# Kernel tuning notes

Measured on AMD Instinct MI355X. Metric: run time of the kernel, lower is better.

Reference implementation:

```python
import jax, jax.numpy as jnp
import numpy as np


def setup_inputs() -> dict:
    key = jax.random.key(0)
    kq, kk, kv = jax.random.split(key, 3)
    B, H, S, D = 2, 8, 2048, 64
    Q = jax.random.normal(kq, (B, H, S, D), dtype=jnp.float32)
    K = jax.random.normal(kk, (B, 1, S, D), dtype=jnp.float32)
    V = jax.random.normal(kv, (B, 1, S, D), dtype=jnp.float32)
    return {"Q": Q, "K": K, "V": V}


def reference(Q, K, V):
    # Multi-query attention: K/V have a single shared head.
    D = Q.shape[-1]
    scale = 1.0 / jnp.sqrt(jnp.asarray(D, dtype=Q.dtype))
    Kh = K[:, 0]  # [B, S, D]
    Vh = V[:, 0]  # [B, S, D]
    # scores: [B, H, Sq, Sk]
    scores = jnp.einsum('bhqd,bkd->bhqk', Q, Kh) * scale
    probs = jax.nn.softmax(scores, axis=-1)
    out = jnp.einsum('bhqk,bkd->bhqd', probs, Vh)  # [B, H, S, D]
    return out
```

## Files before the change

kernel.cpp:

```cpp
#include <hip/hip_runtime.h>
#include <stdint.h>

typedef __attribute__((ext_vector_type(8))) short     bf16x8;
typedef __attribute__((ext_vector_type(4))) float     f32x4;
typedef __attribute__((ext_vector_type(4))) float     float4v;
typedef __attribute__((ext_vector_type(2))) unsigned  uint2v;
typedef __attribute__((ext_vector_type(4))) unsigned  uint4v;

#define DEVINL static __device__ __forceinline__

#define B_  2
#define H_  8
#define S_  2048
#define D_  64
#define KVB 128
#define NKT (S_ / KVB)

DEVINL unsigned short f2bf(float f) {
  union { float f; unsigned u; } v; v.f = f;
  unsigned r = v.u + 0x7FFFu + ((v.u >> 16) & 1u);
  return (unsigned short)(r >> 16);
}

DEVINL void gload_lds16(const void* g, void* l) {
  __builtin_amdgcn_global_load_lds(
      (const __attribute__((address_space(1))) void*)g,
      (__attribute__((address_space(3))) void*)l, 16, 0, 0);
}

__global__ __launch_bounds__(256) void prep_kernel(
    const float* __restrict__ K, const float* __restrict__ V,
    unsigned short* __restrict__ Kb, unsigned short* __restrict__ Vt) {
  const int t = threadIdx.x;
  if (blockIdx.x < 128) {
    const int base = blockIdx.x * 2048 + t * 8;
    const float4v a = *(const float4v*)(K + base);
    const float4v b = *(const float4v*)(K + base + 4);
    uint4v o;
    o.x = (unsigned)f2bf(a.x) | ((unsigned)f2bf(a.y) << 16);
    o.y = (unsigned)f2bf(a.z) | ((unsigned)f2bf(a.w) << 16);
    o.z = (unsigned)f2bf(b.x) | ((unsigned)f2bf(b.y) << 16);
    o.w = (unsigned)f2bf(b.z) | ((unsigned)f2bf(b.w) << 16);
    *(uint4v*)(Kb + base) = o;
  } else {
    __shared__ float Vf[64][65];
    const int vb   = blockIdx.x - 128;
    const int b    = vb >> 5;
    const int sblk = vb & 31;
    const int r = t >> 2, c = t & 3;
    const float* src = V + ((size_t)(b * S_ + sblk * 64 + r)) * 64 + c * 16;
#pragma unroll
    for (int j = 0; j < 4; ++j) {
      float4v x = *(const float4v*)(src + 4 * j);
      Vf[r][c * 16 + 4 * j + 0] = x.x;
      Vf[r][c * 16 + 4 * j + 1] = x.y;
      Vf[r][c * 16 + 4 * j + 2] = x.z;
      Vf[r][c * 16 + 4 * j + 3] = x.w;
    }
    __syncthreads();
    unsigned short o[16];
#pragma unroll
    for (int j = 0; j < 16; ++j) o[j] = f2bf(Vf[c * 16 + j][r]);
    unsigned short* dst = Vt + ((size_t)(b * 64 + r)) * S_ + sblk * 64 + c * 16;
    uint4v w0, w1;
    w0.x = (unsigned)o[0]  | ((unsigned)o[1]  << 16);
    w0.y = (unsigned)o[2]  | ((unsigned)o[3]  << 16);
    w0.z = (unsigned)o[4]  | ((unsigned)o[5]  << 16);
    w0.w = (unsigned)o[6]  | ((unsigned)o[7]  << 16);
    w1.x = (unsigned)o[8]  | ((unsigned)o[9]  << 16);
    w1.y = (unsigned)o[10] | ((unsigned)o[11] << 16);
    w1.z = (unsigned)o[12] | ((unsigned)o[13] << 16);
    w1.w = (unsigned)o[14] | ((unsigned)o[15] << 16);
    *(uint4v*)(dst)     = w0;
    *(uint4v*)(dst + 8) = w1;
  }
}

__global__ __launch_bounds__(256, 2) void attn_kernel(
    const float* __restrict__ Q, const unsigned short* __restrict__ Kb,
    const unsigned short* __restrict__ Vt, float* __restrict__ O) {
  __shared__ __align__(16) unsigned short Klds[2][8192];
  __shared__ __align__(16) unsigned short Vlds[2][8192];
  __shared__ __align__(16) unsigned short Plds[4][2048];

  const int bid = blockIdx.x;
  const int b  = bid >> 8;
  const int h  = (bid >> 5) & 7;
  const int qt = bid & 31;

  const int tid  = threadIdx.x;
  const int lane = tid & 63;
  const int wave = tid >> 6;
  const int g    = lane >> 4;
  const int ql   = lane & 15;
  const int qx   = ql & 7;
  const int gh   = g >> 1;
  const int glo  = g & 1;

  const unsigned short* Kbase = Kb + (size_t)b * (S_ * 64);
  const unsigned short* Vbase = Vt + (size_t)b * (64 * S_);

  const float qscale = 0.125f * 1.4426950408889634f;
  const float* qrow = Q + ((size_t)((b * H_ + h) * S_) + (size_t)(qt * 64 + wave * 16 + ql)) * 64;
  bf16x8 qfrag[2];
#pragma unroll
  for (int s = 0; s < 2; ++s) {
    const float* p = qrow + s * 32 + g * 8;
    float4v x0 = *(const float4v*)(p);
    float4v x1 = *(const float4v*)(p + 4);
    bf16x8 f;
    f[0] = (short)f2bf(x0.x * qscale); f[1] = (short)f2bf(x0.y * qscale);
    f[2] = (short)f2bf(x0.z * qscale); f[3] = (short)f2bf(x0.w * qscale);
    f[4] = (short)f2bf(x1.x * qscale); f[5] = (short)f2bf(x1.y * qscale);
    f[6] = (short)f2bf(x1.z * qscale); f[7] = (short)f2bf(x1.w * qscale);
    qfrag[s] = f;
  }

  bf16x8 ones;
#pragma unroll
  for (int j = 0; j < 8; ++j) ones[j] = (short)0x3F80;

  const int krow   = lane >> 3;
  const int kchunk = (lane & 7) ^ krow;
  const int vrow   = lane >> 4;

  f32x4 acc[4];
#pragma unroll
  for (int nt = 0; nt < 4; ++nt) acc[nt] = (f32x4){0.f, 0.f, 0.f, 0.f};
  f32x4 acc5 = (f32x4){0.f, 0.f, 0.f, 0.f};
  float mrun = -__builtin_inff();

#define STAGE(BUF, KT)                                                                     \
  do {                                                                                     \
    _Pragma("unroll")                                                                      \
    for (int i = 0; i < 4; ++i) {                                                          \
      gload_lds16(Kbase + (size_t)((KT) * KVB + 32 * wave + 8 * i + krow) * 64 + kchunk * 8, \
                  &Klds[BUF][2048 * wave + 512 * i + lane * 8]);                           \
      const int vch = (lane & 15) ^ vrow ^ (4 * (i & 1));                                  \
      gload_lds16(Vbase + (size_t)(16 * wave + 4 * i + vrow) * S_ + (KT) * KVB + vch * 8,  \
                  &Vlds[BUF][2048 * wave + 512 * i + lane * 8]);                           \
    }                                                                                      \
  } while (0)

  STAGE(0, 0);

  int buf = 0;
  for (int kt = 0; kt < NKT; ++kt) {
    __syncthreads();

    if (kt + 1 < NKT) STAGE(buf ^ 1, kt + 1);

    f32x4 sc[8];
#pragma unroll
    for (int mt = 0; mt < 8; ++mt) sc[mt] = (f32x4){0.f, 0.f, 0.f, 0.f};
    __builtin_amdgcn_s_setprio(1);
#pragma unroll
    for (int s = 0; s < 2; ++s) {
#pragma unroll
      for (int mt = 0; mt < 8; ++mt) {
        const bf16x8 a = *(const bf16x8*)&Klds[buf][(mt * 16 + ql) * 64 + ((s * 4 + g) ^ qx) * 8];
        sc[mt] = __builtin_amdgcn_mfma_f32_16x16x32_bf16(a, qfrag[s], sc[mt], 0, 0, 0);
      }
    }
    __builtin_amdgcn_s_setprio(0);

    float mx = fmaxf(fmaxf(sc[0][0], sc[0][1]), fmaxf(sc[0][2], sc[0][3]));
#pragma unroll
    for (int mt = 1; mt < 8; ++mt) {
      const float m0 = fmaxf(fmaxf(sc[mt][0], sc[mt][1]), fmaxf(sc[mt][2], sc[mt][3]));
      mx = fmaxf(mx, m0);
    }
    mx = fmaxf(mx, __shfl_xor(mx, 16));
    mx = fmaxf(mx, __shfl_xor(mx, 32));

    if (!__all(mx <= mrun + 8.f)) {
      const float mnew = fmaxf(mrun, mx);
      const float fac  = __builtin_amdgcn_exp2f(mrun - mnew);
      float facr[4];
#pragma unroll
      for (int r = 0; r < 4; ++r) facr[r] = __shfl(fac, g * 4 + r);
#pragma unroll
      for (int nt = 0; nt < 4; ++nt)
#pragma unroll
        for (int r = 0; r < 4; ++r) acc[nt][r] *= facr[r];
#pragma unroll
      for (int r = 0; r < 4; ++r) acc5[r] *= facr[r];
      mrun = mnew;
    }

#pragma unroll
    for (int mt = 0; mt < 8; ++mt) {
      const float p0 = __builtin_amdgcn_exp2f(sc[mt][0] - mrun);
      const float p1 = __builtin_amdgcn_exp2f(sc[mt][1] - mrun);
      const float p2 = __builtin_amdgcn_exp2f(sc[mt][2] - mrun);
      const float p3 = __builtin_amdgcn_exp2f(sc[mt][3] - mrun);
      uint2v w;
      w.x = (unsigned)f2bf(p0) | ((unsigned)f2bf(p1) << 16);
      w.y = (unsigned)f2bf(p2) | ((unsigned)f2bf(p3) << 16);
      *(uint2v*)&Plds[wave][ql * 128 + ((2 * mt + gh) ^ qx) * 8 + 4 * glo] = w;
    }
    asm volatile("" ::: "memory");

    __builtin_amdgcn_s_setprio(1);
#pragma unroll
    for (int s = 0; s < 4; ++s) {
      const bf16x8 pa = *(const bf16x8*)&Plds[wave][ql * 128 + ((s * 4 + g) ^ qx) * 8];
      acc5 = __builtin_amdgcn_mfma_f32_16x16x32_bf16(pa, ones, acc5, 0, 0, 0);
#pragma unroll
      for (int nt = 0; nt < 4; ++nt) {
        const bf16x8 bv = *(const bf16x8*)&Vlds[buf][(nt * 16 + ql) * 128 + ((s * 4 + g) ^ qx) * 8];
        acc[nt] = __builtin_amdgcn_mfma_f32_16x16x32_bf16(pa, bv, acc[nt], 0, 0, 0);
      }
    }
    __builtin_amdgcn_s_setprio(0);

    buf ^= 1;
  }

  float inv[4];
#pragma unroll
  for (int r = 0; r < 4; ++r) inv[r] = 1.f / acc5[r];
  float* obase = O + ((size_t)((b * H_ + h) * S_) + (size_t)(qt * 64 + wave * 16)) * 64;
#pragma unroll
  for (int nt = 0; nt < 4; ++nt)
#pragma unroll
    for (int r = 0; r < 4; ++r)
      obase[(size_t)(4 * g + r) * 64 + nt * 16 + ql] = acc[nt][r] * inv[r];
}

extern "C" void kernel_launch(void* const* d_in, const int* in_sizes, int n_in,
                              void* d_out, int out_size, void* d_ws, size_t ws_size,
                              hipStream_t stream) {
  const float* Q = (const float*)d_in[0];
  const float* K = (const float*)d_in[1];
  const float* V = (const float*)d_in[2];
  float* O = (float*)d_out;

  unsigned short* Kb = (unsigned short*)d_ws;
  unsigned short* Vt = Kb + (size_t)B_ * S_ * 64;

  prep_kernel<<<192, 256, 0, stream>>>(K, V, Kb, Vt);
  attn_kernel<<<B_ * H_ * (S_ / 64), 256, 0, stream>>>(Q, Kb, Vt, O);
}
```

Before: 46.50 us.

## Pre-swizzle K/V into MFMA fragment order and load directly from global

The prep kernel now writes K and V in bf16 directly in the per-lane MFMA operand order, so each lane's fragment is one contiguous 16-byte chunk. The attention kernel drops the LDS double-buffered staging of K/V and the per-tile __syncthreads, reading fragments straight from global memory (L2/L1 cached), which frees LDS and removes barriers. The risk is exposed global load latency inside the MFMA loop, since there is no explicit prefetch, and repeated global traffic across the 512 blocks that share K/V.

```diff
diff --git a/kernel.cpp b/kernel.cpp
--- a/kernel.cpp
+++ b/kernel.cpp
@@ -22,65 +22,68 @@
   return (unsigned short)(r >> 16);
 }
 
-DEVINL void gload_lds16(const void* g, void* l) {
-  __builtin_amdgcn_global_load_lds(
-      (const __attribute__((address_space(1))) void*)g,
-      (__attribute__((address_space(3))) void*)l, 16, 0, 0);
-}
-
 __global__ __launch_bounds__(256) void prep_kernel(
     const float* __restrict__ K, const float* __restrict__ V,
-    unsigned short* __restrict__ Kb, unsigned short* __restrict__ Vt) {
+    unsigned short* __restrict__ Kf, unsigned short* __restrict__ Vf) {
   const int t = threadIdx.x;
   if (blockIdx.x < 128) {
-    const int base = blockIdx.x * 2048 + t * 8;
-    const float4v a = *(const float4v*)(K + base);
-    const float4v b = *(const float4v*)(K + base + 4);
+    const int gt  = blockIdx.x * 256 + t;
+    const int b   = gt >> 14;
+    const int key = (gt >> 3) & 2047;
+    const int d0  = gt & 7;
+    const int kt  = key >> 7;
+    const int mt  = (key >> 4) & 7;
+    const int ql  = key & 15;
+    const int s   = d0 >> 2;
+    const int g   = d0 & 3;
+    const int lane = g * 16 + ql;
+
+    const float* src = K + ((size_t)(b * 2048 + key)) * 64 + d0 * 8;
+    const float4v x0 = *(const float4v*)(src);
+    const float4v x1 = *(const float4v*)(src + 4);
     uint4v o;
-    o.x = (unsigned)f2bf(a.x) | ((unsigned)f2bf(a.y) << 16);
-    o.y = (unsigned)f2bf(a.z) | ((unsigned)f2bf(a.w) << 16);
-    o.z = (unsigned)f2bf(b.x) | ((unsigned)f2bf(b.y) << 16);
-    o.w = (unsigned)f2bf(b.z) | ((unsigned)f2bf(b.w) << 16);
-    *(uint4v*)(Kb + base) = o;
+    o.x = (unsigned)f2bf(x0.x) | ((unsigned)f2bf(x0.y) << 16);
+    o.y = (unsigned)f2bf(x0.z) | ((unsigned)f2bf(x0.w) << 16);
+    o.z = (unsigned)f2bf(x1.x) | ((unsigned)f2bf(x1.y) << 16);
+    o.w = (unsigned)f2bf(x1.z) | ((unsigned)f2bf(x1.w) << 16);
+    const size_t off = ((size_t)((((b * 16 + kt) * 8 + mt) * 2 + s)) * 64 + lane) * 8;
+    *(uint4v*)(Kf + off) = o;
   } else {
-    __shared__ float Vf[64][65];
-    const int vb   = blockIdx.x - 128;
-    const int b    = vb >> 5;
-    const int sblk = vb & 31;
-    const int r = t >> 2, c = t & 3;
-    const float* src = V + ((size_t)(b * S_ + sblk * 64 + r)) * 64 + c * 16;
-#pragma unroll
-    for (int j = 0; j < 4; ++j) {
-      float4v x = *(const float4v*)(src + 4 * j);
-      Vf[r][c * 16 + 4 * j + 0] = x.x;
-      Vf[r][c * 16 + 4 * j + 1] = x.y;
-      Vf[r][c * 16 + 4 * j + 2] = x.z;
-      Vf[r][c * 16 + 4 * j + 3] = x.w;
-    }
+    __shared__ float Vs[32][65];
+    const int vb = blockIdx.x - 128;
+    const int b  = vb >> 6;
+    const int kt = (vb >> 2) & 15;
+    const int s  = vb & 3;
+
+    const int r  = t >> 3;
+    const int c0 = (t & 7) * 8;
+    const float* src = V + ((size_t)(b * 2048 + kt * 128 + s * 32 + r)) * 64 + c0;
+    const float4v y0 = *(const float4v*)(src);
+    const float4v y1 = *(const float4v*)(src + 4);
+    Vs[r][c0 + 0] = y0.x; Vs[r][c0 + 1] = y0.y; Vs[r][c0 + 2] = y0.z; Vs[r][c0 + 3] = y0.w;
+    Vs[r][c0 + 4] = y1.x; Vs[r][c0 + 5] = y1.y; Vs[r][c0 + 6] = y1.z; Vs[r][c0 + 7] = y1.w;
     __syncthreads();
-    unsigned short o[16];
-#pragma unroll
-    for (int j = 0; j < 16; ++j) o[j] = f2bf(Vf[c * 16 + j][r]);
-    unsigned short* dst = Vt + ((size_t)(b * 64 + r)) * S_ + sblk * 64 + c * 16;
-    uint4v w0, w1;
-    w0.x = (unsigned)o[0]  | ((unsigned)o[1]  << 16);
-    w0.y = (unsigned)o[2]  | ((unsigned)o[3]  << 16);
-    w0.z = (unsigned)o[4]  | ((unsigned)o[5]  << 16);
-    w0.w = (unsigned)o[6]  | ((unsigned)o[7]  << 16);
-    w1.x = (unsigned)o[8]  | ((unsigned)o[9]  << 16);
-    w1.y = (unsigned)o[10] | ((unsigned)o[11] << 16);
-    w1.z = (unsigned)o[12] | ((unsigned)o[13] << 16);
-    w1.w = (unsigned)o[14] | ((unsigned)o[15] << 16);
-    *(uint4v*)(dst)     = w0;
-    *(uint4v*)(dst + 8) = w1;
+
+    const int nt   = t >> 6;
+    const int lane = t & 63;
+    const int g    = lane >> 4;
+    const int ql   = lane & 15;
+    unsigned short o[8];
+#pragma unroll
+    for (int j = 0; j < 8; ++j) o[j] = f2bf(Vs[g * 8 + j][nt * 16 + ql]);
+    uint4v w;
+    w.x = (unsigned)o[0] | ((unsigned)o[1] << 16);
+    w.y = (unsigned)o[2] | ((unsigned)o[3] << 16);
+    w.z = (unsigned)o[4] | ((unsigned)o[5] << 16);
+    w.w = (unsigned)o[6] | ((unsigned)o[7] << 16);
+    const size_t off = ((size_t)((((b * 16 + kt) * 4 + s)) * 4 + nt) * 64 + lane) * 8;
+    *(uint4v*)(Vf + off) = w;
   }
 }
 
 __global__ __launch_bounds__(256, 2) void attn_kernel(
-    const float* __restrict__ Q, const unsigned short* __restrict__ Kb,
-    const unsigned short* __restrict__ Vt, float* __restrict__ O) {
-  __shared__ __align__(16) unsigned short Klds[2][8192];
-  __shared__ __align__(16) unsigned short Vlds[2][8192];
+    const float* __restrict__ Q, const unsigned short* __restrict__ Kf,
+    const unsigned short* __restrict__ Vf, float* __restrict__ O) {
   __shared__ __align__(16) unsigned short Plds[4][2048];
 
   const int bid = blockIdx.x;
@@ -97,8 +100,8 @@
   const int gh   = g >> 1;
   const int glo  = g & 1;
 
-  const unsigned short* Kbase = Kb + (size_t)b * (S_ * 64);
-  const unsigned short* Vbase = Vt + (size_t)b * (64 * S_);
+  const unsigned short* Kb = Kf + (size_t)b * (NKT * 8 * 2 * 512);
+  const unsigned short* Vb = Vf + (size_t)b * (NKT * 4 * 4 * 512);
 
   const float qscale = 0.125f * 1.4426950408889634f;
   const float* qrow = Q + ((size_t)((b * H_ + h) * S_) + (size_t)(qt * 64 + wave * 16 + ql)) * 64;
@@ -120,35 +123,15 @@
 #pragma unroll
   for (int j = 0; j < 8; ++j) ones[j] = (short)0x3F80;
 
-  const int krow   = lane >> 3;
-  const int kchunk = (lane & 7) ^ krow;
-  const int vrow   = lane >> 4;
-
   f32x4 acc[4];
 #pragma unroll
   for (int nt = 0; nt < 4; ++nt) acc[nt] = (f32x4){0.f, 0.f, 0.f, 0.f};
   f32x4 acc5 = (f32x4){0.f, 0.f, 0.f, 0.f};
   float mrun = -__builtin_inff();
 
-#define STAGE(BUF, KT)                                                                     \
-  do {                                                                                     \
-    _Pragma("unroll")                                                                      \
-    for (int i = 0; i < 4; ++i) {                                                          \
-      gload_lds16(Kbase + (size_t)((KT) * KVB + 32 * wave + 8 * i + krow) * 64 + kchunk * 8, \
-                  &Klds[BUF][2048 * wave + 512 * i + lane * 8]);                           \
-      const int vch = (lane & 15) ^ vrow ^ (4 * (i & 1));                                  \
-      gload_lds16(Vbase + (size_t)(16 * wave + 4 * i + vrow) * S_ + (KT) * KVB + vch * 8,  \
-                  &Vlds[BUF][2048 * wave + 512 * i + lane * 8]);                           \
-    }                                                                                      \
-  } while (0)
-
-  STAGE(0, 0);
-
-  int buf = 0;
   for (int kt = 0; kt < NKT; ++kt) {
-    __syncthreads();
-
-    if (kt + 1 < NKT) STAGE(buf ^ 1, kt + 1);
+    const unsigned short* Kt = Kb + (size_t)kt * 8192;
+    const unsigned short* Vt = Vb + (size_t)kt * 8192;
 
     f32x4 sc[8];
 #pragma unroll
@@ -158,7 +141,7 @@
     for (int s = 0; s < 2; ++s) {
 #pragma unroll
       for (int mt = 0; mt < 8; ++mt) {
-        const bf16x8 a = *(const bf16x8*)&Klds[buf][(mt * 16 + ql) * 64 + ((s * 4 + g) ^ qx) * 8];
+        const bf16x8 a = *(const bf16x8*)(Kt + (mt * 2 + s) * 512 + lane * 8);
         sc[mt] = __builtin_amdgcn_mfma_f32_16x16x32_bf16(a, qfrag[s], sc[mt], 0, 0, 0);
       }
     }
@@ -208,13 +191,11 @@
       acc5 = __builtin_amdgcn_mfma_f32_16x16x32_bf16(pa, ones, acc5, 0, 0, 0);
 #pragma unroll
       for (int nt = 0; nt < 4; ++nt) {
-        const bf16x8 bv = *(const bf16x8*)&Vlds[buf][(nt * 16 + ql) * 128 + ((s * 4 + g) ^ qx) * 8];
+        const bf16x8 bv = *(const bf16x8*)(Vt + (s * 4 + nt) * 512 + lane * 8);
         acc[nt] = __builtin_amdgcn_mfma_f32_16x16x32_bf16(pa, bv, acc[nt], 0, 0, 0);
       }
     }
     __builtin_amdgcn_s_setprio(0);
-
-    buf ^= 1;
   }
 
   float inv[4];
@@ -236,9 +217,9 @@
   const float* V = (const float*)d_in[2];
   float* O = (float*)d_out;
 
-  unsigned short* Kb = (unsigned short*)d_ws;
-  unsigned short* Vt = Kb + (size_t)B_ * S_ * 64;
-
-  prep_kernel<<<192, 256, 0, stream>>>(K, V, Kb, Vt);
-  attn_kernel<<<B_ * H_ * (S_ / 64), 256, 0, stream>>>(Q, Kb, Vt, O);
-}
+  unsigned short* Kf = (unsigned short*)d_ws;
+  unsigned short* Vf = Kf + (size_t)B_ * NKT * 8 * 2 * 512;
+
+  prep_kernel<<<256, 256, 0, stream>>>(K, V, Kf, Vf);
+  attn_kernel<<<B_ * H_ * (S_ / 64), 256, 0, stream>>>(Q, Kf, Vf, O);
+}
```

Measured after the change: 67.07 us. 1.44x slower.

## Switch attention to 32x32x16 MFMA with split-KV waves and register P

Applied to the files above, without the earlier changes.

Replaces the 16x16x32 MFMA tiling with 32x32x16 MFMAs, so each wave handles 32 query rows against half of each 128-key tile (split-KV across wave pairs), merged at the end through LDS with a log-sum-exp combine. The P matrix is kept in registers and reshuffled across lanes instead of being written to and read back from LDS, and the row sum is computed with VALU adds instead of an extra MFMA against a ones vector. The aim is fewer LDS round trips and MFMA issues per tile. In exchange the kernel needs more accumulator registers, a cross-lane shuffle per P fragment, and an epilogue reduction with extra barriers.

```diff
diff --git a/kernel.cpp b/kernel.cpp
--- a/kernel.cpp
+++ b/kernel.cpp
@@ -1,11 +1,10 @@
 #include <hip/hip_runtime.h>
 #include <stdint.h>
 
-typedef __attribute__((ext_vector_type(8))) short     bf16x8;
-typedef __attribute__((ext_vector_type(4))) float     f32x4;
-typedef __attribute__((ext_vector_type(4))) float     float4v;
-typedef __attribute__((ext_vector_type(2))) unsigned  uint2v;
-typedef __attribute__((ext_vector_type(4))) unsigned  uint4v;
+typedef __attribute__((ext_vector_type(8)))  short    bf16x8;
+typedef __attribute__((ext_vector_type(16))) float    f32x16;
+typedef __attribute__((ext_vector_type(4)))  float    float4v;
+typedef __attribute__((ext_vector_type(4)))  unsigned uint4v;
 
 #define DEVINL static __device__ __forceinline__
 
@@ -22,11 +21,23 @@
   return (unsigned short)(r >> 16);
 }
 
+DEVINL unsigned pk2(float a, float b) {
+  return (unsigned)f2bf(a) | ((unsigned)f2bf(b) << 16);
+}
+
 DEVINL void gload_lds16(const void* g, void* l) {
   __builtin_amdgcn_global_load_lds(
       (const __attribute__((address_space(1))) void*)g,
       (__attribute__((address_space(3))) void*)l, 16, 0, 0);
 }
+
+DEVINL bf16x8 frag_from_words(unsigned a, unsigned b, unsigned c, unsigned d) {
+  union { unsigned u[4]; bf16x8 v; } x;
+  x.u[0] = a; x.u[1] = b; x.u[2] = c; x.u[3] = d;
+  return x.v;
+}
+
+#define CROW(r, hi) (((r) & 3) + 8 * ((r) >> 2) + 4 * (hi))
 
 __global__ __launch_bounds__(256) void prep_kernel(
     const float* __restrict__ K, const float* __restrict__ V,
@@ -79,9 +90,7 @@
 __global__ __launch_bounds__(256, 2) void attn_kernel(
     const float* __restrict__ Q, const unsigned short* __restrict__ Kb,
     const unsigned short* __restrict__ Vt, float* __restrict__ O) {
-  __shared__ __align__(16) unsigned short Klds[2][8192];
-  __shared__ __align__(16) unsigned short Vlds[2][8192];
-  __shared__ __align__(16) unsigned short Plds[4][2048];
+  __shared__ __align__(16) unsigned char smem[65536];
 
   const int bid = blockIdx.x;
   const int b  = bid >> 8;
@@ -91,21 +100,21 @@
   const int tid  = threadIdx.x;
   const int lane = tid & 63;
   const int wave = tid >> 6;
-  const int g    = lane >> 4;
-  const int ql   = lane & 15;
-  const int qx   = ql & 7;
-  const int gh   = g >> 1;
-  const int glo  = g & 1;
+  const int qg   = wave & 1;
+  const int kh   = wave >> 1;
+  const int hi   = lane >> 5;
+  const int lq   = lane & 31;
+  const int l7   = lane & 7;
 
   const unsigned short* Kbase = Kb + (size_t)b * (S_ * 64);
   const unsigned short* Vbase = Vt + (size_t)b * (64 * S_);
 
   const float qscale = 0.125f * 1.4426950408889634f;
-  const float* qrow = Q + ((size_t)((b * H_ + h) * S_) + (size_t)(qt * 64 + wave * 16 + ql)) * 64;
-  bf16x8 qfrag[2];
-#pragma unroll
-  for (int s = 0; s < 2; ++s) {
-    const float* p = qrow + s * 32 + g * 8;
+  const float* qrow = Q + ((size_t)((b * H_ + h) * S_) + (size_t)(qt * 64 + qg * 32 + lq)) * 64;
+  bf16x8 qfrag[4];
+#pragma unroll
+  for (int ks = 0; ks < 4; ++ks) {
+    const float* p = qrow + ks * 16 + hi * 8;
     float4v x0 = *(const float4v*)(p);
     float4v x1 = *(const float4v*)(p + 4);
     bf16x8 f;
@@ -113,33 +122,35 @@
     f[2] = (short)f2bf(x0.z * qscale); f[3] = (short)f2bf(x0.w * qscale);
     f[4] = (short)f2bf(x1.x * qscale); f[5] = (short)f2bf(x1.y * qscale);
     f[6] = (short)f2bf(x1.z * qscale); f[7] = (short)f2bf(x1.w * qscale);
-    qfrag[s] = f;
-  }
-
-  bf16x8 ones;
-#pragma unroll
-  for (int j = 0; j < 8; ++j) ones[j] = (short)0x3F80;
+    qfrag[ks] = f;
+  }
 
   const int krow   = lane >> 3;
   const int kchunk = (lane & 7) ^ krow;
   const int vrow   = lane >> 4;
 
-  f32x4 acc[4];
-#pragma unroll
-  for (int nt = 0; nt < 4; ++nt) acc[nt] = (f32x4){0.f, 0.f, 0.f, 0.f};
-  f32x4 acc5 = (f32x4){0.f, 0.f, 0.f, 0.f};
+  f32x16 acc0, acc1;
+#pragma unroll
+  for (int r = 0; r < 16; ++r) { acc0[r] = 0.f; acc1[r] = 0.f; }
   float mrun = -__builtin_inff();
-
-#define STAGE(BUF, KT)                                                                     \
-  do {                                                                                     \
-    _Pragma("unroll")                                                                      \
-    for (int i = 0; i < 4; ++i) {                                                          \
-      gload_lds16(Kbase + (size_t)((KT) * KVB + 32 * wave + 8 * i + krow) * 64 + kchunk * 8, \
-                  &Klds[BUF][2048 * wave + 512 * i + lane * 8]);                           \
-      const int vch = (lane & 15) ^ vrow ^ (4 * (i & 1));                                  \
-      gload_lds16(Vbase + (size_t)(16 * wave + 4 * i + vrow) * S_ + (KT) * KVB + vch * 8,  \
-                  &Vlds[BUF][2048 * wave + 512 * i + lane * 8]);                           \
-    }                                                                                      \
+  float lrun = 0.f;
+
+#define KL(BUF) ((unsigned short*)(smem + (BUF) * 16384))
+#define VL(BUF) ((unsigned short*)(smem + 32768 + (BUF) * 16384))
+
+#define STAGE(BUF, KT)                                                                   \
+  do {                                                                                   \
+    _Pragma("unroll")                                                                    \
+    for (int i = 0; i < 4; ++i) {                                                        \
+      const int kj = wave * 4 + i;                           \
+      gload_lds16(Kbase + (size_t)((KT) * KVB + kj * 8 + krow) * 64 + kchunk * 8,        \
+                  KL(BUF) + kj * 512 + lane * 8);                                        \
+      const int vj = wave * 4 + i;                         \
+      const int vr = vj * 4 + vrow;                                                      \
+      const int vch = (lane & 15) ^ (vr & 7);                                            \
+      gload_lds16(Vbase + (size_t)vr * S_ + (KT) * KVB + vch * 8,                        \
+                  VL(BUF) + vj * 512 + lane * 8);                                        \
+    }                                                                                    \
   } while (0)
 
   STAGE(0, 0);
@@ -150,82 +161,113 @@
 
     if (kt + 1 < NKT) STAGE(buf ^ 1, kt + 1);
 
-    f32x4 sc[8];
-#pragma unroll
-    for (int mt = 0; mt < 8; ++mt) sc[mt] = (f32x4){0.f, 0.f, 0.f, 0.f};
+    f32x16 c0, c1;
+#pragma unroll
+    for (int r = 0; r < 16; ++r) { c0[r] = 0.f; c1[r] = 0.f; }
+    const unsigned short* Kt = KL(buf);
     __builtin_amdgcn_s_setprio(1);
 #pragma unroll
-    for (int s = 0; s < 2; ++s) {
-#pragma unroll
-      for (int mt = 0; mt < 8; ++mt) {
-        const bf16x8 a = *(const bf16x8*)&Klds[buf][(mt * 16 + ql) * 64 + ((s * 4 + g) ^ qx) * 8];
-        sc[mt] = __builtin_amdgcn_mfma_f32_16x16x32_bf16(a, qfrag[s], sc[mt], 0, 0, 0);
-      }
+    for (int ks = 0; ks < 4; ++ks) {
+      const int ch = (2 * ks + hi) ^ l7;
+      const bf16x8 a0 = *(const bf16x8*)(Kt + (kh * 64 + lq) * 64 + ch * 8);
+      c0 = __builtin_amdgcn_mfma_f32_32x32x16_bf16(a0, qfrag[ks], c0, 0, 0, 0);
+      const bf16x8 a1 = *(const bf16x8*)(Kt + (kh * 64 + 32 + lq) * 64 + ch * 8);
+      c1 = __builtin_amdgcn_mfma_f32_32x32x16_bf16(a1, qfrag[ks], c1, 0, 0, 0);
     }
     __builtin_amdgcn_s_setprio(0);
 
-    float mx = fmaxf(fmaxf(sc[0][0], sc[0][1]), fmaxf(sc[0][2], sc[0][3]));
-#pragma unroll
-    for (int mt = 1; mt < 8; ++mt) {
-      const float m0 = fmaxf(fmaxf(sc[mt][0], sc[mt][1]), fmaxf(sc[mt][2], sc[mt][3]));
-      mx = fmaxf(mx, m0);
-    }
-    mx = fmaxf(mx, __shfl_xor(mx, 16));
+    float mx = fmaxf(c0[0], c0[1]);
+#pragma unroll
+    for (int r = 2; r < 16; ++r) mx = fmaxf(mx, c0[r]);
+#pragma unroll
+    for (int r = 0; r < 16; ++r) mx = fmaxf(mx, c1[r]);
     mx = fmaxf(mx, __shfl_xor(mx, 32));
 
     if (!__all(mx <= mrun + 8.f)) {
       const float mnew = fmaxf(mrun, mx);
       const float fac  = __builtin_amdgcn_exp2f(mrun - mnew);
-      float facr[4];
-#pragma unroll
-      for (int r = 0; r < 4; ++r) facr[r] = __shfl(fac, g * 4 + r);
-#pragma unroll
-      for (int nt = 0; nt < 4; ++nt)
-#pragma unroll
-        for (int r = 0; r < 4; ++r) acc[nt][r] *= facr[r];
-#pragma unroll
-      for (int r = 0; r < 4; ++r) acc5[r] *= facr[r];
+#pragma unroll
+      for (int r = 0; r < 16; ++r) {
+        const float fr = __shfl(fac, CROW(r, hi));
+        acc0[r] *= fr; acc1[r] *= fr;
+      }
+      lrun *= fac;
       mrun = mnew;
     }
 
-#pragma unroll
-    for (int mt = 0; mt < 8; ++mt) {
-      const float p0 = __builtin_amdgcn_exp2f(sc[mt][0] - mrun);
-      const float p1 = __builtin_amdgcn_exp2f(sc[mt][1] - mrun);
-      const float p2 = __builtin_amdgcn_exp2f(sc[mt][2] - mrun);
-      const float p3 = __builtin_amdgcn_exp2f(sc[mt][3] - mrun);
-      uint2v w;
-      w.x = (unsigned)f2bf(p0) | ((unsigned)f2bf(p1) << 16);
-      w.y = (unsigned)f2bf(p2) | ((unsigned)f2bf(p3) << 16);
-      *(uint2v*)&Plds[wave][ql * 128 + ((2 * mt + gh) ^ qx) * 8 + 4 * glo] = w;
-    }
-    asm volatile("" ::: "memory");
-
-    __builtin_amdgcn_s_setprio(1);
-#pragma unroll
-    for (int s = 0; s < 4; ++s) {
-      const bf16x8 pa = *(const bf16x8*)&Plds[wave][ql * 128 + ((s * 4 + g) ^ qx) * 8];
-      acc5 = __builtin_amdgcn_mfma_f32_16x16x32_bf16(pa, ones, acc5, 0, 0, 0);
-#pragma unroll
-      for (int nt = 0; nt < 4; ++nt) {
-        const bf16x8 bv = *(const bf16x8*)&Vlds[buf][(nt * 16 + ql) * 128 + ((s * 4 + g) ^ qx) * 8];
-        acc[nt] = __builtin_amdgcn_mfma_f32_16x16x32_bf16(pa, bv, acc[nt], 0, 0, 0);
-      }
-    }
-    __builtin_amdgcn_s_setprio(0);
+    float psum = 0.f;
+#pragma unroll
+    for (int r = 0; r < 16; ++r) {
+      c0[r] = __builtin_amdgcn_exp2f(c0[r] - mrun);
+      c1[r] = __builtin_amdgcn_exp2f(c1[r] - mrun);
+      psum += c0[r] + c1[r];
+    }
+    psum += __shfl_xor(psum, 32);
+    lrun += psum;
+
+    const unsigned short* Vb = VL(buf);
+#pragma unroll
+    for (int ks = 0; ks < 4; ++ks) {
+      const int e = ks & 1;
+      const f32x16 ct = (ks >> 1) ? c1 : c0;
+      const unsigned wx0 = pk2(ct[8 * e + 0], ct[8 * e + 1]);
+      const unsigned wx1 = pk2(ct[8 * e + 2], ct[8 * e + 3]);
+      const unsigned wy0 = pk2(ct[8 * e + 4], ct[8 * e + 5]);
+      const unsigned wy1 = pk2(ct[8 * e + 6], ct[8 * e + 7]);
+      const unsigned s0 = hi ? wx0 : wy0;
+      const unsigned s1 = hi ? wx1 : wy1;
+      const unsigned r0 = (unsigned)__shfl_xor((int)s0, 32);
+      const unsigned r1 = (unsigned)__shfl_xor((int)s1, 32);
+      const bf16x8 pfrag = frag_from_words(hi ? r0 : wx0, hi ? r1 : wx1,
+                                           hi ? wy0 : r0, hi ? wy1 : r1);
+      const int ch = (kh * 8) | ((2 * ks + hi) ^ l7);
+      __builtin_amdgcn_s_setprio(1);
+      const bf16x8 bv0 = *(const bf16x8*)(Vb + (size_t)lq * 128 + ch * 8);
+      acc0 = __builtin_amdgcn_mfma_f32_32x32x16_bf16(pfrag, bv0, acc0, 0, 0, 0);
+      const bf16x8 bv1 = *(const bf16x8*)(Vb + (size_t)(32 + lq) * 128 + ch * 8);
+      acc1 = __builtin_amdgcn_mfma_f32_32x32x16_bf16(pfrag, bv1, acc1, 0, 0, 0);
+      __builtin_amdgcn_s_setprio(0);
+    }
 
     buf ^= 1;
   }
 
-  float inv[4];
-#pragma unroll
-  for (int r = 0; r < 4; ++r) inv[r] = 1.f / acc5[r];
-  float* obase = O + ((size_t)((b * H_ + h) * S_) + (size_t)(qt * 64 + wave * 16)) * 64;
-#pragma unroll
-  for (int nt = 0; nt < 4; ++nt)
-#pragma unroll
-    for (int r = 0; r < 4; ++r)
-      obase[(size_t)(4 * g + r) * 64 + nt * 16 + ql] = acc[nt][r] * inv[r];
+  __syncthreads();
+  float* Mbuf = (float*)(smem + 16384);
+  float* Lbuf = (float*)(smem + 16384 + 512);
+  float* Abuf = (float*)(smem + 32768);
+  if (lane < 32) {
+    Mbuf[(qg * 2 + kh) * 32 + lane] = mrun;
+    Lbuf[(qg * 2 + kh) * 32 + lane] = lrun;
+  }
+  __syncthreads();
+  const float mo = Mbuf[(qg * 2 + (kh ^ 1)) * 32 + lq];
+  const float lo = Lbuf[(qg * 2 + (kh ^ 1)) * 32 + lq];
+  const float mtot  = fmaxf(mrun, mo);
+  const float sself = __builtin_amdgcn_exp2f(mrun - mtot);
+  const float ltot  = lrun * sself + lo * __builtin_amdgcn_exp2f(mo - mtot);
+
+  if (kh == 1) {
+#pragma unroll
+    for (int r = 0; r < 16; ++r) {
+      const float sr = __shfl(sself, CROW(r, hi));
+      Abuf[qg * 2048 + CROW(r, hi) * 64 + lq]      = acc0[r] * sr;
+      Abuf[qg * 2048 + CROW(r, hi) * 64 + 32 + lq] = acc1[r] * sr;
+    }
+  }
+  __syncthreads();
+  if (kh == 0) {
+    const float linv = 1.f / ltot;
+    float* obase = O + ((size_t)((b * H_ + h) * S_) + (size_t)(qt * 64 + qg * 32)) * 64;
+#pragma unroll
+    for (int r = 0; r < 16; ++r) {
+      const float sr = __shfl(sself, CROW(r, hi));
+      const float iv = __shfl(linv,  CROW(r, hi));
+      const int row  = CROW(r, hi);
+      obase[(size_t)row * 64 + lq]      = (acc0[r] * sr + Abuf[qg * 2048 + row * 64 + lq]) * iv;
+      obase[(size_t)row * 64 + 32 + lq] = (acc1[r] * sr + Abuf[qg * 2048 + row * 64 + 32 + lq]) * iv;
+    }
+  }
 }
 
 extern "C" void kernel_launch(void* const* d_in, const int* in_sizes, int n_in,
```

Measured after the change: 47.10 us. No clear change (+1.3%).
